# Performance work log

Hardware: AMD Instinct MI355X
Metric: run time of the kernel (lower is better)

## Reference

```python
import jax, jax.numpy as jnp
import numpy as np

B, N, D, R, W, H, I = 256, 2048, 128, 4, 1, 1024, 1024
CI = I + R * D                       # controller input size (1536)
IF = 2 * D * W + 2 * W + 1 + 4 * R + D * R   # interface size (787)
OPI = H + R * D                      # output_proj input (1536)


def _norm(v):
    # F.normalize(dim=-1): x / max(||x||, eps)
    return v / jnp.maximum(jnp.linalg.norm(v, axis=-1, keepdims=True), 1e-12)


def setup_inputs() -> dict:
    key = jax.random.key(0)
    ks = jax.random.split(key, 16)
    u = lambda k, shape, fan: jax.random.uniform(k, shape, jnp.float32, -1.0 / np.sqrt(fan), 1.0 / np.sqrt(fan))
    return {
        "x": jax.random.normal(ks[0], (B, I), jnp.float32),
        "memory": jax.random.normal(ks[1], (N, D), jnp.float32) * np.sqrt(2.0 / (N + D)),  # xavier-ish
        "usage": jax.random.uniform(ks[2], (N,), jnp.float32),          # usage in [0,1)
        "link": jax.random.normal(ks[3], (N, N), jnp.float32) * 0.01,   # non-trivial link state
        "W_ih": u(ks[4], (4 * H, CI), H),
        "W_hh": u(ks[5], (4 * H, H), H),
        "b_ih": u(ks[6], (4 * H,), H),
        "b_hh": u(ks[7], (4 * H,), H),
        "W_if": u(ks[8], (IF, H), H),
        "b_if": u(ks[9], (IF,), H),
        "W_out": u(ks[10], (H, OPI), OPI),
        "b_out": u(ks[11], (H,), OPI),
    }


def reference(x, memory, usage, link, W_ih, W_hh, b_ih, b_hh, W_if, b_if, W_out, b_out):
    # initial uniform read weights (prev state at first step)
    prev_rw = jnp.full((B, R, N), 1.0 / N, x.dtype)
    read_flat = (prev_rw @ memory).reshape(B, -1)                 # (B, R*D)
    cin = jnp.concatenate([x, read_flat], axis=-1)                # (B, CI)

    # single LSTM step, h0 = c0 = 0, torch gate order i,f,g,o
    g = cin @ W_ih.T + b_ih + b_hh
    gi, gf, gg, go = jnp.split(g, 4, axis=-1)
    c = jax.nn.sigmoid(gi) * jnp.tanh(gg)
    h = jax.nn.sigmoid(go) * jnp.tanh(c)                          # (B, H) controller out

    itf = h @ W_if.T + b_if                                       # (B, IF)
    o = 0
    write_vals = itf[:, o:o + D * W].reshape(B, W, D); o += D * W
    erase = jax.nn.sigmoid(itf[:, o:o + D * W]).reshape(B, W, D); o += D * W
    write_gates = jax.nn.sigmoid(itf[:, o:o + W]); o += W         # (B, W)
    alloc_gate = jax.nn.sigmoid(itf[:, o:o + 1]); o += 1          # (B, 1)
    o += W                                                        # free gates (parsed, unused)
    read_modes = jax.nn.softmax(itf[:, o:o + 3 * R].reshape(B, R, 3), -1); o += 3 * R
    read_str = jax.nn.softplus(itf[:, o:o + R]); o += R           # (B, R)
    read_keys = itf[:, o:o + D * R].reshape(B, R, D)

    # content addressing for the write (strength = 1)
    mem_n = _norm(memory)
    cw = jax.nn.softmax(_norm(write_vals.mean(1)) @ mem_n.T, -1)  # (B, N)

    # allocation weighting: sorted-usage cumprod (per source semantics)
    idx = jnp.argsort(usage)
    su = usage[idx]
    cp = jnp.cumprod(1.0 - su)
    alloc_s = jnp.concatenate([su[:1], su[1:] * cp[:-1]])
    alloc = jnp.zeros_like(usage).at[idx].set(alloc_s)[None, :] * alloc_gate  # (B, N)

    write_w = write_gates[:, :, None] * (0.5 * cw + 0.5 * alloc)[:, None, :]  # (B, W, N)

    # temporal link update: batch-mean of diag-masked outer product, decay 0.9
    lu = jnp.einsum('bwn,bwm->nm', write_w, write_w) / B
    lu = lu * (1.0 - jnp.eye(N, dtype=lu.dtype))
    link_new = link * 0.9 + lu * 0.1

    # memory write (erase then add, batch-mean)
    ev = erase * write_gates[:, :, None]
    av = write_vals * write_gates[:, :, None]
    erase_mat = jnp.einsum('bwn,bwd->nd', write_w, ev) / B
    add_mat = jnp.einsum('bwn,bwd->nd', write_w, av) / B
    mem_new = memory * (1.0 - erase_mat) + add_mat

    # read addressing on updated memory and updated link (all R heads vectorized)
    sim = jnp.einsum('brd,nd->brn', _norm(read_keys), _norm(mem_new))
    content_r = jax.nn.softmax(sim * read_str[:, :, None], -1)    # (B, R, N)
    backward_w = jnp.einsum('brn,nm->brm', prev_rw, link_new)     # mode 1: prev @ L
    forward_w = jnp.einsum('brn,mn->brm', prev_rw, link_new)      # mode 2: prev @ L^T
    new_rw = (read_modes[..., 0:1] * content_r
              + read_modes[..., 1:2] * backward_w
              + read_modes[..., 2:3] * forward_w)                 # (B, R, N)

    read_out = (new_rw @ mem_new).reshape(B, -1)                  # (B, R*D)
    out = jnp.concatenate([h, read_out], axis=-1) @ W_out.T + b_out
    return out
```

## Files before the change

kernel.cpp:

```cpp
#include <hip/hip_runtime.h>
#include <cmath>

#define DEVI __device__ __forceinline__

DEVI float sigm(float x){ return 1.f/(1.f+expf(-x)); }

typedef __attribute__((ext_vector_type(8))) _Float16 half8;
typedef __attribute__((ext_vector_type(4))) _Float16 half4;
typedef __attribute__((ext_vector_type(4))) float float4v;


__global__ void k_zero(float* __restrict__ p, int n){
  int i = blockIdx.x*256 + threadIdx.x;
  if (i < n) p[i] = 0.f;
}

__global__ __launch_bounds__(256) void k_stage1(
    const float* __restrict__ mem, float* __restrict__ cm, _Float16* __restrict__ mem_h,
    const float* __restrict__ usage, float* __restrict__ alloc, float* __restrict__ Sa,
    const float* __restrict__ link, float* __restrict__ rsl, float* __restrict__ csl)
{
  __shared__ float smem[4][132];
  const int blk = blockIdx.x, t = threadIdx.x;
  const int wv = t >> 6, lane = t & 63;

  if (blk < 32){
    int n0 = blk*64;
    float c0 = 0.f, c1 = 0.f;
    for (int r = wv; r < 64; r += 4){
      const float* a = mem + (size_t)(n0+r)*128;
      float x0 = a[lane], x1 = a[lane+64];
      float ss = x0*x0 + x1*x1;
      #pragma unroll
      for (int o = 1; o < 64; o <<= 1) ss += __shfl_xor(ss, o);
      float invn = 1.f / fmaxf(sqrtf(ss), 1e-12f);
      mem_h[(size_t)(n0+r)*128 + lane]      = (_Float16)(x0*invn);
      mem_h[(size_t)(n0+r)*128 + 64 + lane] = (_Float16)(x1*invn);
      c0 += x0; c1 += x1;
    }
    smem[wv][lane] = c0; smem[wv][64+lane] = c1;
    __syncthreads();
    if (t < 128) atomicAdd(&cm[t], smem[0][t]+smem[1][t]+smem[2][t]+smem[3][t]);
  } else if (blk < 2080){
    int n = blk - 32;
    float un = usage[n];
    float prod = 1.f;
    #pragma unroll
    for (int i = 0; i < 8; i++){
      int m = t + i*256;
      float um = usage[m];
      bool before = (um < un) || (um == un && m < n);
      prod *= before ? (1.f - um) : 1.f;
    }
    #pragma unroll
    for (int o = 32; o > 0; o >>= 1) prod *= __shfl_xor(prod, o);
    if (lane == 0) smem[0][wv] = prod;
    __syncthreads();
    if (t == 0){
      float v = un * (smem[0][0]*smem[0][1]) * (smem[0][2]*smem[0][3]);
      alloc[n] = v;
      atomicAdd(Sa, v);
    }
  } else {
    int r0 = (blk - 2080)*32;
    int c0 = t*8;
    float colacc[8];
    #pragma unroll
    for (int j = 0; j < 8; j++) colacc[j] = 0.f;
    for (int rg = 0; rg < 32; rg += 4){
      float4v v0[4], v1[4];
      #pragma unroll
      for (int u = 0; u < 4; u++){
        const float* lp = link + (size_t)(r0+rg+u)*2048 + c0;
        v0[u] = *(const float4v*)lp;
        v1[u] = *(const float4v*)(lp+4);
      }
      #pragma unroll
      for (int u = 0; u < 4; u++){
        float s = 0.f;
        #pragma unroll
        for (int j = 0; j < 4; j++){
          colacc[j]   += v0[u][j]; colacc[4+j] += v1[u][j];
          s += v0[u][j] + v1[u][j];
        }
        #pragma unroll
        for (int o = 32; o > 0; o >>= 1) s += __shfl_xor(s, o);
        if (lane == 0) smem[wv][rg+u] = s;
      }
    }
    __syncthreads();
    if (t < 32) rsl[r0+t] = smem[0][t]+smem[1][t]+smem[2][t]+smem[3][t];
    #pragma unroll
    for (int j = 0; j < 8; j++) atomicAdd(&csl[c0+j], colacc[j]);
  }
}

__global__ void k_cin(const float* __restrict__ x, const float* __restrict__ cm, _Float16* __restrict__ cin){
  int idx = blockIdx.x*256 + threadIdx.x;
  int b = idx / 1536, k = idx - b*1536;
  float v = (k < 1024) ? x[b*1024 + k] : cm[(k-1024) & 127] * (1.f/2048.f);
  cin[idx] = (_Float16)v;
}

__global__ void k_lstm(const float* __restrict__ g, _Float16* __restrict__ h){
  int idx = blockIdx.x*256 + threadIdx.x;
  int b = idx >> 10, j = idx & 1023;
  const float* gr = g + (size_t)b*4096;
  float c = sigm(gr[j]) * tanhf(gr[2048 + j]);
  h[idx] = (_Float16)(sigm(gr[3072 + j]) * tanhf(c));
}

#define QA 264
#define QB 520

template<typename TB> struct BReg;
template<> struct BReg<_Float16>{
  half8 v;
  DEVI void load(const _Float16* p){ v = *(const half8*)p; }
  DEVI half8 get() const { return v; }
};
template<> struct BReg<float>{
  float4v a, b;
  DEVI void load(const float* p){ a = *(const float4v*)p; b = *(const float4v*)(p+4); }
  DEVI half8 get() const {
    half8 h;
    #pragma unroll
    for (int j = 0; j < 4; j++){ h[j] = (_Float16)a[j]; h[4+j] = (_Float16)b[j]; }
    return h;
  }
};

template<typename TB>
__global__ __launch_bounds__(256) void gemm_t(
    const _Float16* __restrict__ A, const TB* __restrict__ Bm, float* __restrict__ C,
    int M, int N, int K,
    const float* __restrict__ bias1, const float* __restrict__ bias2)
{
  __shared__ _Float16 Ah[2][8*QA];
  __shared__ _Float16 Bh[2][8*QB];
  const int tid = threadIdx.x;
  const int m0 = blockIdx.y*32, n0 = blockIdx.x*64;
  const int T = K >> 6;
  const int arow = tid >> 3, aq = tid & 7;
  const int brow = tid >> 3, bq = tid & 7;
  int nB0 = n0 + brow;      if (nB0 >= N) nB0 = N - 1;
  int nB1 = n0 + brow + 32; if (nB1 >= N) nB1 = N - 1;
  const _Float16* Aptr = A + (size_t)(m0 + arow)*K + aq*8;
  const TB* Bp0 = Bm + (size_t)nB0*K + bq*8;
  const TB* Bp1 = Bm + (size_t)nB1*K + bq*8;
  const int wA  = aq*QA + arow*8;
  const int wB0 = bq*QB + brow*8;
  const int wB1 = bq*QB + (brow+32)*8;
  const int wv_ = tid >> 6, lane = tid & 63;
  const int fq = lane >> 4, fr = lane & 15;
  const int m16 = (wv_ & 1)*16, nb = (wv_ >> 1)*32;

  half8 ra;
  BReg<TB> rb0, rb1;
  ra = *(const half8*)(Aptr);
  rb0.load(Bp0);
  rb1.load(Bp1);
  *(half8*)&Ah[0][wA]  = ra;
  *(half8*)&Bh[0][wB0] = rb0.get();
  *(half8*)&Bh[0][wB1] = rb1.get();
  __syncthreads();

  float4v acc0 = {0.f,0.f,0.f,0.f}, acc1 = {0.f,0.f,0.f,0.f};
  for (int t = 0; t < T; t++){
    const int cur = t & 1, nxt = cur ^ 1;
    if (t+1 < T){
      ra = *(const half8*)(Aptr + (t+1)*64);
      rb0.load(Bp0 + (t+1)*64);
      rb1.load(Bp1 + (t+1)*64);
    }
    #pragma unroll
    for (int s = 0; s < 2; s++){
      int q = s*4 + fq;
      half8 a  = *(half8*)&Ah[cur][q*QA + (m16+fr)*8];
      half8 b0 = *(half8*)&Bh[cur][q*QB + (nb+fr)*8];
      half8 b1 = *(half8*)&Bh[cur][q*QB + (nb+16+fr)*8];
      acc0 = __builtin_amdgcn_mfma_f32_16x16x32_f16(a, b0, acc0, 0, 0, 0);
      acc1 = __builtin_amdgcn_mfma_f32_16x16x32_f16(a, b1, acc1, 0, 0, 0);
    }
    if (t+1 < T){
      *(half8*)&Ah[nxt][wA]  = ra;
      *(half8*)&Bh[nxt][wB0] = rb0.get();
      *(half8*)&Bh[nxt][wB1] = rb1.get();
    }
    __syncthreads();
  }

  const int colA = n0 + nb + fr, colB = colA + 16;
  #pragma unroll
  for (int i = 0; i < 4; i++){
    int m = m0 + m16 + fq*4 + i;
    if (colA < N){
      float v = acc0[i];
      if (bias1) v += bias1[colA];
      if (bias2) v += bias2[colA];
      C[(size_t)m*N + colA] = v;
    }
    if (colB < N){
      float v = acc1[i];
      if (bias1) v += bias1[colB];
      if (bias2) v += bias2[colB];
      C[(size_t)m*N + colB] = v;
    }
  }
}

DEVI float blockReduce128(float v, float* lds2){
  #pragma unroll
  for (int o = 32; o > 0; o >>= 1) v += __shfl_xor(v, o);
  int w = threadIdx.x >> 6;
  __syncthreads();
  if ((threadIdx.x & 63) == 0) lds2[w] = v;
  __syncthreads();
  return lds2[0] + lds2[1];
}

__global__ __launch_bounds__(128) void k_parse(const float* __restrict__ itf,
    _Float16* __restrict__ wv_h, float* __restrict__ ev, float* __restrict__ av,
    float* __restrict__ wg_, float* __restrict__ ag_,
    float* __restrict__ rm0, float* __restrict__ rm1, float* __restrict__ rm2,
    _Float16* __restrict__ rks_h)
{
  __shared__ float red[2];
  int b = blockIdx.x, t = threadIdx.x;
  const float* it = itf + (size_t)b*787;
  float wg = sigm(it[256]);
  float ag = sigm(it[257]);
  if (t == 0){ wg_[b] = wg; ag_[b] = ag; }
  float w = it[t];
  av[b*128 + t] = w * wg;
  ev[b*128 + t] = sigm(it[128 + t]) * wg;
  float ss = blockReduce128(w*w, red);
  float invwv = 1.f / fmaxf(sqrtf(ss), 1e-12f);
  wv_h[b*128 + t] = (_Float16)(w * invwv);
  if (t < 4){
    int rr = t;
    float m0v = it[259 + rr*3 + 0], m1v = it[259 + rr*3 + 1], m2v = it[259 + rr*3 + 2];
    float mx = fmaxf(m0v, fmaxf(m1v, m2v));
    float e0 = expf(m0v - mx), e1 = expf(m1v - mx), e2 = expf(m2v - mx);
    float inv = 1.f / (e0 + e1 + e2);
    rm0[b*4 + rr] = e0*inv; rm1[b*4 + rr] = e1*inv; rm2[b*4 + rr] = e2*inv;
  }
  #pragma unroll
  for (int rr = 0; rr < 4; rr++){
    float kv = it[275 + rr*128 + t];
    float ks = blockReduce128(kv*kv, red);
    float sx = it[271 + rr];
    float str = fmaxf(sx, 0.f) + log1pf(expf(-fabsf(sx)));
    float invk = 1.f / fmaxf(sqrtf(ks), 1e-12f);
    rks_h[((size_t)b*4 + rr)*128 + t] = (_Float16)(kv * invk * str);
  }
}

__global__ __launch_bounds__(256) void k_softmax_ww(float* __restrict__ P,
    const float* __restrict__ alloc, const float* __restrict__ wg, const float* __restrict__ ag){
  __shared__ float red[4];
  float* p = P + (size_t)blockIdx.x*2048;
  int t = threadIdx.x;
  float r[8];
  float mx = -3.4e38f;
  #pragma unroll
  for (int i = 0; i < 8; i++){ r[i] = p[t + i*256]; mx = fmaxf(mx, r[i]); }
  #pragma unroll
  for (int o = 32; o > 0; o >>= 1) mx = fmaxf(mx, __shfl_xor(mx, o));
  if ((t & 63) == 0) red[t >> 6] = mx;
  __syncthreads();
  mx = fmaxf(fmaxf(red[0], red[1]), fmaxf(red[2], red[3]));
  float s = 0.f;
  #pragma unroll
  for (int i = 0; i < 8; i++){ r[i] = expf(r[i] - mx); s += r[i]; }
  #pragma unroll
  for (int o = 32; o > 0; o >>= 1) s += __shfl_xor(s, o);
  __syncthreads();
  if ((t & 63) == 0) red[t >> 6] = s;
  __syncthreads();
  s = red[0] + red[1] + red[2] + red[3];
  float inv = 1.f / s;
  float wgb = wg[blockIdx.x], agb = ag[blockIdx.x];
  #pragma unroll
  for (int i = 0; i < 8; i++){
    int col = t + i*256;
    p[col] = wgb*(0.5f*r[i]*inv + 0.5f*alloc[col]*agb);
  }
}

__global__ __launch_bounds__(256) void k_bwfw(const float* __restrict__ ww,
                       const float* __restrict__ wg, const float* __restrict__ ag,
                       const float* __restrict__ Sa,
                       const float* __restrict__ rowsum, const float* __restrict__ colsum,
                       float* __restrict__ bw, float* __restrict__ fw){
  __shared__ float sq[4][64], sd[4][64];
  __shared__ float tbs[256];
  int t = threadIdx.x & 63, z = threadIdx.x >> 6;
  int m = blockIdx.x*64 + t;
  {
    float sa = Sa[0];
    int b = threadIdx.x;
    tbs[b] = wg[b]*(0.5f + 0.5f*ag[b]*sa);
  }
  __syncthreads();
  float q = 0.f, dd = 0.f;
  for (int b = z*64; b < z*64 + 64; b += 4){
    float w0 = ww[(size_t)(b+0)*2048 + m];
    float w1 = ww[(size_t)(b+1)*2048 + m];
    float w2 = ww[(size_t)(b+2)*2048 + m];
    float w3 = ww[(size_t)(b+3)*2048 + m];
    q  = fmaf(tbs[b+0], w0, q);  dd = fmaf(w0, w0, dd);
    q  = fmaf(tbs[b+1], w1, q);  dd = fmaf(w1, w1, dd);
    q  = fmaf(tbs[b+2], w2, q);  dd = fmaf(w2, w2, dd);
    q  = fmaf(tbs[b+3], w3, q);  dd = fmaf(w3, w3, dd);
  }
  sq[z][t] = q; sd[z][t] = dd;
  __syncthreads();
  if (z == 0){
    q  = sq[0][t] + sq[1][t] + sq[2][t] + sq[3][t];
    dd = sd[0][t] + sd[1][t] + sd[2][t] + sd[3][t];
    float lus = (q - dd) * (1.f/256.f);
    bw[m] = (0.9f*colsum[m] + 0.1f*lus) * (1.f/2048.f);
    fw[m] = (0.9f*rowsum[m] + 0.1f*lus) * (1.f/2048.f);
  }
}

__global__ __launch_bounds__(256) void k_memupdate_fused(const float* __restrict__ ww,
    const float* __restrict__ ev, const float* __restrict__ av,
    const float* __restrict__ mem, const float* __restrict__ bw, const float* __restrict__ fw,
    _Float16* __restrict__ memn_h, _Float16* __restrict__ memnT_h,
    float* __restrict__ bwm, float* __restrict__ fwm)
{
  __shared__ float Ws[16][34];
  __shared__ float Es[16][132], Vs[16][132];
  __shared__ float lb[128], lf[128];
  __shared__ _Float16 Traw[32][132];
  const int n0 = blockIdx.x*32;
  const int tid = threadIdx.x, tx = tid & 31, ty = tid >> 5;
  if (tid < 128){ lb[tid] = 0.f; lf[tid] = 0.f; }
  const int wk = tid >> 4, wn = (tid & 15)*2;
  const int ek = tid >> 4, ec = (tid & 15)*8;
  float ae[4][4] = {}, aa[4][4] = {};
  for (int k0 = 0; k0 < 256; k0 += 16){
    float2 vw  = *(const float2*)(ww + (size_t)(k0+wk)*2048 + n0 + wn);
    float4 ve0 = *(const float4*)(ev + (size_t)(k0+ek)*128 + ec);
    float4 ve1 = *(const float4*)(ev + (size_t)(k0+ek)*128 + ec + 4);
    float4 va0 = *(const float4*)(av + (size_t)(k0+ek)*128 + ec);
    float4 va1 = *(const float4*)(av + (size_t)(k0+ek)*128 + ec + 4);
    __syncthreads();
    Ws[wk][wn] = vw.x; Ws[wk][wn+1] = vw.y;
    *(float4*)&Es[ek][ec] = ve0; *(float4*)&Es[ek][ec+4] = ve1;
    *(float4*)&Vs[ek][ec] = va0; *(float4*)&Vs[ek][ec+4] = va1;
    __syncthreads();
    #pragma unroll
    for (int k = 0; k < 16; k++){
      float a[4], e[4], v[4];
      #pragma unroll
      for (int i = 0; i < 4; i++) a[i] = Ws[k][ty*4+i];
      #pragma unroll
      for (int j = 0; j < 4; j++){ e[j] = Es[k][tx*4+j]; v[j] = Vs[k][tx*4+j]; }
      #pragma unroll
      for (int i = 0; i < 4; i++)
        #pragma unroll
        for (int j = 0; j < 4; j++){
          ae[i][j] = fmaf(a[i], e[j], ae[i][j]);
          aa[i][j] = fmaf(a[i], v[j], aa[i][j]);
        }
    }
  }
  float ab[4] = {0,0,0,0}, af[4] = {0,0,0,0};
  #pragma unroll
  for (int i = 0; i < 4; i++){
    int n = n0 + ty*4 + i;
    float bwn = bw[n], fwn = fw[n];
    float v[4]; float ss = 0.f;
    #pragma unroll
    for (int j = 0; j < 4; j++){
      int d = tx*4 + j;
      float em = ae[i][j]*(1.f/256.f), am = aa[i][j]*(1.f/256.f);
      float mv = mem[(size_t)n*128 + d]*(1.f - em) + am;
      v[j] = mv; ss += mv*mv;
      ab[j] = fmaf(bwn, mv, ab[j]);
      af[j] = fmaf(fwn, mv, af[j]);
    }
    #pragma unroll
    for (int o = 1; o < 32; o <<= 1) ss += __shfl_xor(ss, o);
    float invn = 1.f / fmaxf(sqrtf(ss), 1e-12f);
    half4 hn, hr;
    #pragma unroll
    for (int j = 0; j < 4; j++){ hn[j] = (_Float16)(v[j]*invn); hr[j] = (_Float16)v[j]; }
    *(half4*)(memn_h + (size_t)n*128 + tx*4) = hn;
    *(half4*)&Traw[ty*4+i][tx*4] = hr;
  }
  __syncthreads();
  {
    int d = tid >> 1, seg = (tid & 1)*16;
    half8 o0, o1;
    #pragma unroll
    for (int j = 0; j < 8; j++){ o0[j] = Traw[seg+j][d]; o1[j] = Traw[seg+8+j][d]; }
    *(half8*)(memnT_h + (size_t)d*2048 + n0 + seg)     = o0;
    *(half8*)(memnT_h + (size_t)d*2048 + n0 + seg + 8) = o1;
  }
  #pragma unroll
  for (int j = 0; j < 4; j++){
    atomicAdd(&lb[tx*4+j], ab[j]);
    atomicAdd(&lf[tx*4+j], af[j]);
  }
  __syncthreads();
  if (tid < 128){
    atomicAdd(&bwm[tid], lb[tid]);
    atomicAdd(&fwm[tid], lf[tid]);
  }
}

__global__ __launch_bounds__(256) void k_flash(
    const _Float16* __restrict__ Q, const _Float16* __restrict__ Kh,
    const _Float16* __restrict__ Vt,
    float* __restrict__ pacc, float* __restrict__ pm, float* __restrict__ pl)
{
  __shared__ _Float16 Pl[4][16][32];
  __shared__ float cmb[4][2080];
  __shared__ float scl[4][16];
  const int tid = threadIdx.x;
  const int qt = blockIdx.x >> 2, kc = blockIdx.x & 3;
  const int wv = tid >> 6, lane = tid & 63;
  const int fq = lane >> 4, fr = lane & 15;
  const int kw0 = kc*512 + wv*128;

  half8 aq[4];
  #pragma unroll
  for (int c = 0; c < 4; c++)
    aq[c] = *(const half8*)(Q + (size_t)(qt*16 + fr)*128 + c*32 + fq*8);

  float m[4] = {-3.0e38f,-3.0e38f,-3.0e38f,-3.0e38f};
  float l[4] = {0.f,0.f,0.f,0.f};
  float4v acc[8] = {};
  for (int s = 0; s < 4; s++){
    const int kb = kw0 + s*32;
    float4v S0 = {0,0,0,0}, S1 = {0,0,0,0};
    #pragma unroll
    for (int c = 0; c < 4; c++){
      half8 b0 = *(const half8*)(Kh + (size_t)(kb + fr)*128      + c*32 + fq*8);
      half8 b1 = *(const half8*)(Kh + (size_t)(kb + 16 + fr)*128 + c*32 + fq*8);
      S0 = __builtin_amdgcn_mfma_f32_16x16x32_f16(aq[c], b0, S0, 0, 0, 0);
      S1 = __builtin_amdgcn_mfma_f32_16x16x32_f16(aq[c], b1, S1, 0, 0, 0);
    }
    float mt[4], ps[4];
    #pragma unroll
    for (int i = 0; i < 4; i++) mt[i] = fmaxf(S0[i], S1[i]);
    #pragma unroll
    for (int o = 1; o < 16; o <<= 1){
      #pragma unroll
      for (int i = 0; i < 4; i++) mt[i] = fmaxf(mt[i], __shfl_xor(mt[i], o));
    }
    #pragma unroll
    for (int i = 0; i < 4; i++){
      float mn = fmaxf(m[i], mt[i]);
      float al = expf(m[i] - mn);
      float p0 = expf(S0[i] - mn), p1 = expf(S1[i] - mn);
      S0[i] = p0; S1[i] = p1;
      ps[i] = p0 + p1;
      l[i] *= al;
      m[i] = mn;
      #pragma unroll
      for (int c = 0; c < 8; c++) acc[c][i] *= al;
    }
    #pragma unroll
    for (int o = 1; o < 16; o <<= 1){
      #pragma unroll
      for (int i = 0; i < 4; i++) ps[i] += __shfl_xor(ps[i], o);
    }
    #pragma unroll
    for (int i = 0; i < 4; i++) l[i] += ps[i];
    #pragma unroll
    for (int i = 0; i < 4; i++){
      Pl[wv][fq*4+i][fr]      = (_Float16)S0[i];
      Pl[wv][fq*4+i][16 + fr] = (_Float16)S1[i];
    }
    half8 pf = *(half8*)&Pl[wv][fr][fq*8];
    #pragma unroll
    for (int c = 0; c < 8; c++){
      half8 bv = *(const half8*)(Vt + (size_t)(c*16 + fr)*2048 + kb + fq*8);
      acc[c] = __builtin_amdgcn_mfma_f32_16x16x32_f16(pf, bv, acc[c], 0, 0, 0);
    }
  }
  if (fr == 0){
    #pragma unroll
    for (int i = 0; i < 4; i++){
      cmb[wv][fq*4+i]      = m[i];
      cmb[wv][16 + fq*4+i] = l[i];
    }
  }
  #pragma unroll
  for (int c = 0; c < 8; c++)
    #pragma unroll
    for (int i = 0; i < 4; i++)
      cmb[wv][32 + (fq*4+i)*128 + c*16 + fr] = acc[c][i];
  __syncthreads();
  if (tid < 16){
    float mm = fmaxf(fmaxf(cmb[0][tid], cmb[1][tid]), fmaxf(cmb[2][tid], cmb[3][tid]));
    float ll = 0.f;
    #pragma unroll
    for (int w = 0; w < 4; w++){
      float e = expf(cmb[w][tid] - mm);
      scl[w][tid] = e;
      ll += e * cmb[w][16 + tid];
    }
    pm[blockIdx.x*16 + tid] = mm;
    pl[blockIdx.x*16 + tid] = ll;
  }
  __syncthreads();
  for (int e = tid; e < 2048; e += 256){
    int q = e >> 7;
    float a = scl[0][q]*cmb[0][32+e] + scl[1][q]*cmb[1][32+e]
            + scl[2][q]*cmb[2][32+e] + scl[3][q]*cmb[3][32+e];
    pacc[(size_t)blockIdx.x*2048 + e] = a;
  }
}

__global__ void k_hro_comb(const _Float16* __restrict__ h, const float* __restrict__ pacc,
                           const float* __restrict__ pm, const float* __restrict__ pl,
                           const float* __restrict__ rm0, const float* __restrict__ rm1,
                           const float* __restrict__ rm2, const float* __restrict__ bwm,
                           const float* __restrict__ fwm, _Float16* __restrict__ hro){
  int idx = blockIdx.x*256 + threadIdx.x;
  int b = idx / 1536, k = idx - b*1536;
  if (k < 1024){
    hro[idx] = h[b*1024 + k];
  } else {
    int r = k - 1024, rh = r >> 7, d = r & 127;
    int row = b*4 + rh, qt = row >> 4, q = row & 15;
    float mm = -3.0e38f;
    #pragma unroll
    for (int kc = 0; kc < 4; kc++) mm = fmaxf(mm, pm[(qt*4+kc)*16 + q]);
    float num = 0.f, den = 0.f;
    #pragma unroll
    for (int kc = 0; kc < 4; kc++){
      float e = expf(pm[(qt*4+kc)*16 + q] - mm);
      den += e * pl[(qt*4+kc)*16 + q];
      num += e * pacc[(size_t)(qt*4+kc)*2048 + q*128 + d];
    }
    float pv = num / den;
    hro[idx] = (_Float16)(rm0[row]*pv + rm1[row]*bwm[d] + rm2[row]*fwm[d]);
  }
}


extern "C" void kernel_launch(void* const* d_in, const int* in_sizes, int n_in,
                              void* d_out, int out_size, void* d_ws, size_t ws_size,
                              hipStream_t stream)
{
  const float* x     = (const float*)d_in[0];
  const float* mem   = (const float*)d_in[1];
  const float* usage = (const float*)d_in[2];
  const float* link  = (const float*)d_in[3];
  const float* W_ih  = (const float*)d_in[4];
  const float* b_ih  = (const float*)d_in[6];
  const float* b_hh  = (const float*)d_in[7];
  const float* W_if  = (const float*)d_in[8];
  const float* b_if  = (const float*)d_in[9];
  const float* W_out = (const float*)d_in[10];
  const float* b_out = (const float*)d_in[11];
  float* out = (float*)d_out;
  float* ws  = (float*)d_ws;

  float* cm     = ws + 0;
  float* csl    = ws + 128;
  float* bwm    = ws + 2176;
  float* fwm    = ws + 2304;
  float* Sa     = ws + 2432;
  float* bw     = ws + 2688;
  float* fw     = ws + 4736;
  float* wg     = ws + 6784;
  float* ag     = ws + 7040;
  float* rm0    = ws + 7296;
  float* rm1    = ws + 8320;
  float* rm2    = ws + 9344;
  float* alloc  = ws + 10368;
  float* rsl    = ws + 12416;
  float* ev     = ws + 14464;
  float* av     = ws + 47232;
  float* g      = ws + 80000;
  float* itf    = ws + 1128576;
  float* ww     = ws + 1330048;
  float* pacc   = ws + 1854336;
  float* pm     = ws + 2378624;
  float* pl     = ws + 2382720;
  _Float16* wv_h    = (_Float16*)(ws + 2386816);
  _Float16* mem_h   = (_Float16*)(ws + 2403200);
  _Float16* memn_h  = (_Float16*)(ws + 2534272);
  _Float16* memnT_h = (_Float16*)(ws + 2665344);
  _Float16* rks_h   = (_Float16*)(ws + 2796416);
  _Float16* hro_h   = (_Float16*)(ws + 2861952);
  _Float16* cin_h   = (_Float16*)(ws + 3058560);
  _Float16* h_h     = (_Float16*)(ws + 3255168);

  k_zero<<<10, 256, 0, stream>>>(ws, 2433);

  k_stage1<<<2144, 256, 0, stream>>>(mem, cm, mem_h, usage, alloc, Sa, link, rsl, csl);
  k_cin   <<<1536, 256, 0, stream>>>(x, cm, cin_h);

  gemm_t<float><<<dim3(64,8), 256, 0, stream>>>(cin_h, W_ih, g, 256, 4096, 1536, b_ih, b_hh);
  k_lstm<<<1024, 256, 0, stream>>>(g, h_h);

  gemm_t<float><<<dim3(13,8), 256, 0, stream>>>(h_h, W_if, itf, 256, 787, 1024, b_if, nullptr);
  k_parse<<<256, 128, 0, stream>>>(itf, wv_h, ev, av, wg, ag, rm0, rm1, rm2, rks_h);

  gemm_t<_Float16><<<dim3(32,8), 256, 0, stream>>>(wv_h, mem_h, ww, 256, 2048, 128, nullptr, nullptr);
  k_softmax_ww<<<256, 256, 0, stream>>>(ww, alloc, wg, ag);

  k_bwfw<<<32, 256, 0, stream>>>(ww, wg, ag, Sa, rsl, csl, bw, fw);

  k_memupdate_fused<<<64, 256, 0, stream>>>(ww, ev, av, mem, bw, fw, memn_h, memnT_h, bwm, fwm);

  k_flash<<<256, 256, 0, stream>>>(rks_h, memn_h, memnT_h, pacc, pm, pl);

  k_hro_comb<<<1536, 256, 0, stream>>>(h_h, pacc, pm, pl, rm0, rm1, rm2, bwm, fwm, hro_h);
  gemm_t<float><<<dim3(16,8), 256, 0, stream>>>(hro_h, W_out, out, 256, 1024, 1536, b_out, nullptr);

  (void)in_sizes; (void)n_in; (void)out_size; (void)ws_size;
}
```

Measured before the change: 266.2 us.

## Compute alloc per wave, drop Sa atomic, recompute sum in bwfw, rebalance link blocks

The allocation weighting now gives one wavefront per memory slot instead of a full 256-thread block per slot, which cuts the stage-1 grid from 2144 to 672 blocks. The global atomic sum Sa is removed. Each k_bwfw block instead re-reduces the 2048 alloc values itself. The link row/column-sum section now uses 16 rows per block across 128 blocks, up from 32 rows across 64, to spread that work more widely. The cost is redundant alloc summation in all 32 bwfw blocks and more column atomics on csl.

New measurement: 269.2 us. About the same (+1.1%).

```diff
diff --git a/kernel.cpp b/kernel.cpp
--- a/kernel.cpp
+++ b/kernel.cpp
@@ -17,7 +17,7 @@
 
 __global__ __launch_bounds__(256) void k_stage1(
     const float* __restrict__ mem, float* __restrict__ cm, _Float16* __restrict__ mem_h,
-    const float* __restrict__ usage, float* __restrict__ alloc, float* __restrict__ Sa,
+    const float* __restrict__ usage, float* __restrict__ alloc,
     const float* __restrict__ link, float* __restrict__ rsl, float* __restrict__ csl)
 {
   __shared__ float smem[4][132];
@@ -41,33 +41,13 @@
     smem[wv][lane] = c0; smem[wv][64+lane] = c1;
     __syncthreads();
     if (t < 128) atomicAdd(&cm[t], smem[0][t]+smem[1][t]+smem[2][t]+smem[3][t]);
-  } else if (blk < 2080){
-    int n = blk - 32;
-    float un = usage[n];
-    float prod = 1.f;
-    #pragma unroll
-    for (int i = 0; i < 8; i++){
-      int m = t + i*256;
-      float um = usage[m];
-      bool before = (um < un) || (um == un && m < n);
-      prod *= before ? (1.f - um) : 1.f;
-    }
-    #pragma unroll
-    for (int o = 32; o > 0; o >>= 1) prod *= __shfl_xor(prod, o);
-    if (lane == 0) smem[0][wv] = prod;
-    __syncthreads();
-    if (t == 0){
-      float v = un * (smem[0][0]*smem[0][1]) * (smem[0][2]*smem[0][3]);
-      alloc[n] = v;
-      atomicAdd(Sa, v);
-    }
-  } else {
-    int r0 = (blk - 2080)*32;
+  } else if (blk < 160){
+    int r0 = (blk - 32)*16;
     int c0 = t*8;
     float colacc[8];
     #pragma unroll
     for (int j = 0; j < 8; j++) colacc[j] = 0.f;
-    for (int rg = 0; rg < 32; rg += 4){
+    for (int rg = 0; rg < 16; rg += 4){
       float4v v0[4], v1[4];
       #pragma unroll
       for (int u = 0; u < 4; u++){
@@ -89,9 +69,23 @@
       }
     }
     __syncthreads();
-    if (t < 32) rsl[r0+t] = smem[0][t]+smem[1][t]+smem[2][t]+smem[3][t];
+    if (t < 16) rsl[r0+t] = smem[0][t]+smem[1][t]+smem[2][t]+smem[3][t];
     #pragma unroll
     for (int j = 0; j < 8; j++) atomicAdd(&csl[c0+j], colacc[j]);
+  } else {
+    int n = (blk - 160)*4 + wv;
+    float un = usage[n];
+    float prod = 1.f;
+    #pragma unroll
+    for (int i = 0; i < 32; i++){
+      int m = lane + i*64;
+      float um = usage[m];
+      bool before = (um < un) || (um == un && m < n);
+      prod *= before ? (1.f - um) : 1.f;
+    }
+    #pragma unroll
+    for (int o = 32; o > 0; o >>= 1) prod *= __shfl_xor(prod, o);
+    if (lane == 0) alloc[n] = un * prod;
   }
 }
 
@@ -290,18 +284,23 @@
 
 __global__ __launch_bounds__(256) void k_bwfw(const float* __restrict__ ww,
                        const float* __restrict__ wg, const float* __restrict__ ag,
-                       const float* __restrict__ Sa,
+                       const float* __restrict__ alloc,
                        const float* __restrict__ rowsum, const float* __restrict__ colsum,
                        float* __restrict__ bw, float* __restrict__ fw){
   __shared__ float sq[4][64], sd[4][64];
+  __shared__ float sred[4];
   __shared__ float tbs[256];
   int t = threadIdx.x & 63, z = threadIdx.x >> 6;
   int m = blockIdx.x*64 + t;
-  {
-    float sa = Sa[0];
-    int b = threadIdx.x;
-    tbs[b] = wg[b]*(0.5f + 0.5f*ag[b]*sa);
-  }
+  float sa = 0.f;
+  #pragma unroll
+  for (int i = 0; i < 8; i++) sa += alloc[threadIdx.x + i*256];
+  #pragma unroll
+  for (int o = 32; o > 0; o >>= 1) sa += __shfl_xor(sa, o);
+  if (t == 0) sred[z] = sa;
+  __syncthreads();
+  sa = (sred[0]+sred[1]) + (sred[2]+sred[3]);
+  tbs[threadIdx.x] = wg[threadIdx.x]*(0.5f + 0.5f*ag[threadIdx.x]*sa);
   __syncthreads();
   float q = 0.f, dd = 0.f;
   for (int b = z*64; b < z*64 + 64; b += 4){
@@ -568,7 +567,6 @@
   float* csl    = ws + 128;
   float* bwm    = ws + 2176;
   float* fwm    = ws + 2304;
-  float* Sa     = ws + 2432;
   float* bw     = ws + 2688;
   float* fw     = ws + 4736;
   float* wg     = ws + 6784;
@@ -595,9 +593,9 @@
   _Float16* cin_h   = (_Float16*)(ws + 3058560);
   _Float16* h_h     = (_Float16*)(ws + 3255168);
 
-  k_zero<<<10, 256, 0, stream>>>(ws, 2433);
-
-  k_stage1<<<2144, 256, 0, stream>>>(mem, cm, mem_h, usage, alloc, Sa, link, rsl, csl);
+  k_zero<<<10, 256, 0, stream>>>(ws, 2432);
+
+  k_stage1<<<672, 256, 0, stream>>>(mem, cm, mem_h, usage, alloc, link, rsl, csl);
   k_cin   <<<1536, 256, 0, stream>>>(x, cm, cin_h);
 
   gemm_t<float><<<dim3(64,8), 256, 0, stream>>>(cin_h, W_ih, g, 256, 4096, 1536, b_ih, b_hh);
@@ -609,7 +607,7 @@
   gemm_t<_Float16><<<dim3(32,8), 256, 0, stream>>>(wv_h, mem_h, ww, 256, 2048, 128, nullptr, nullptr);
   k_softmax_ww<<<256, 256, 0, stream>>>(ww, alloc, wg, ag);
 
-  k_bwfw<<<32, 256, 0, stream>>>(ww, wg, ag, Sa, rsl, csl, bw, fw);
+  k_bwfw<<<32, 256, 0, stream>>>(ww, wg, ag, alloc, rsl, csl, bw, fw);
 
   k_memupdate_fused<<<64, 256, 0, stream>>>(ww, ev, av, mem, bw, fw, memn_h, memnT_h, bwm, fwm);
 
```
